# Performance work log

Measured on AMD Instinct MI355X. Metric: run time of the kernel, lower is better.

Reference implementation:

```python
import jax, jax.numpy as jnp
import numpy as np

B, N, V, H, R, A, IN, K = 64, 512, 64, 512, 4, 18, 128, 32
EPS = 1e-8


def setup_inputs() -> dict:
    key = jax.random.key(0)
    ks = jax.random.split(key, 20)
    g = lambda i, shape, s=1.0: jax.random.normal(ks[i], shape, jnp.float32) * s
    u = lambda i, shape: jax.random.uniform(ks[i], shape, dtype=jnp.float32)
    cin = IN + R * V
    return dict(
        x=g(0, (B, IN)),
        h=g(1, (B, H), 0.1),
        c=g(2, (B, H), 0.1),
        memory=g(3, (B, N, V), 0.1),
        read_weights=u(4, (B, R, N)),
        write_weights=u(5, (B, N)),
        usage=u(6, (B, N)),
        link_matrix=u(7, (B, N, N)) * 0.01,
        precedence_weights=u(8, (B, N)),
        W_ih=g(9, (4 * H, cin), 0.05), W_hh=g(10, (4 * H, H), 0.05),
        b_ih=jnp.zeros(4 * H, jnp.float32), b_hh=jnp.zeros(4 * H, jnp.float32),
        W_read=g(11, (R, V + 4, H), 0.05), b_read=jnp.zeros((R, V + 4), jnp.float32),
        W_write=g(12, (3 * V + 3, H), 0.05), b_write=jnp.zeros(3 * V + 3, jnp.float32),
        W_pol=g(13, (A, H), 0.05), b_pol=jnp.zeros(A, jnp.float32),
        W_val=g(14, (1, H), 0.05), b_val=jnp.zeros(1, jnp.float32),
    )


def reference(x, h, c, memory, read_weights, write_weights, usage, link_matrix,
              precedence_weights, W_ih, W_hh, b_ih, b_hh, W_read, b_read,
              W_write, b_write, W_pol, b_pol, W_val, b_val):
    # ---- read heads (vectorized over R) ----
    ro = jnp.einsum('roh,bh->bro', W_read, h) + b_read            # [B,R,V+4]
    rkey = ro[..., :V]
    rbeta = jax.nn.softplus(ro[..., V])                           # [B,R]
    rpi = jax.nn.softmax(ro[..., V + 1:V + 4], axis=-1)           # backward/content/forward gates
    mem_norm = jnp.maximum(jnp.linalg.norm(memory, axis=-1), EPS)  # [B,N]
    key_norm = jnp.maximum(jnp.linalg.norm(rkey, axis=-1), EPS)    # [B,R]
    sim = jnp.einsum('bnv,brv->brn', memory, rkey) / (mem_norm[:, None, :] * key_norm[..., None])
    scores = rbeta[..., None] * sim                                # [B,R,N]
    kth = jax.lax.top_k(scores, K)[0][..., -1:]                    # sparse top-k mask
    cw = jax.nn.softmax(jnp.where(scores >= kth, scores, -jnp.inf), axis=-1)
    fw = jnp.einsum('bnm,brm->brn', link_matrix, read_weights)     # forward weighting L w
    bw = jnp.einsum('bmn,brm->brn', link_matrix, read_weights)     # backward weighting L^T w
    w_r = rpi[..., 0:1] * bw + rpi[..., 1:2] * cw + rpi[..., 2:3] * fw  # [B,R,N]
    rvec = jnp.einsum('brn,bnv->brv', w_r, memory).reshape(B, R * V)
    # ---- LSTM controller (torch LSTMCell gate order i,f,g,o) ----
    gates = jnp.concatenate([x, rvec], -1) @ W_ih.T + h @ W_hh.T + b_ih + b_hh
    i_g, f_g, g_g, o_g = jnp.split(gates, 4, axis=-1)
    c_new = jax.nn.sigmoid(f_g) * c + jax.nn.sigmoid(i_g) * jnp.tanh(g_g)
    h_new = jax.nn.sigmoid(o_g) * jnp.tanh(c_new)
    # ---- write head ----
    wo = h_new @ W_write.T + b_write                               # [B,3V+3]
    wkey = wo[:, :V]
    erase = jax.nn.sigmoid(wo[:, V:2 * V])
    add = jnp.tanh(wo[:, 2 * V:3 * V])
    wbeta = jax.nn.softplus(wo[:, 3 * V])
    g_a = jax.nn.sigmoid(wo[:, 3 * V + 1])
    g_w = jax.nn.sigmoid(wo[:, 3 * V + 2])
    wkey_norm = jnp.maximum(jnp.linalg.norm(wkey, axis=-1), EPS)
    wsim = jnp.einsum('bnv,bv->bn', memory, wkey) / (mem_norm * wkey_norm[:, None])
    cw_w = jax.nn.softmax(wbeta[:, None] * wsim, axis=-1)
    # allocation weighting from sorted usage (DNC Eq. 1)
    idx = jnp.argsort(usage, axis=-1)
    u_sorted = jnp.take_along_axis(usage, idx, -1)
    prod_prev = jnp.concatenate([jnp.ones((B, 1), usage.dtype), jnp.cumprod(u_sorted, -1)[:, :-1]], -1)
    a_sorted = (1.0 - u_sorted) * prod_prev
    alloc = jnp.take_along_axis(a_sorted, jnp.argsort(idx, -1), -1)
    write_w = g_w[:, None] * (g_a[:, None] * alloc + (1.0 - g_a)[:, None] * cw_w)  # [B,N]
    # ---- memory erase/add ----
    mem_new = memory * (1.0 - write_w[:, :, None] * erase[:, None, :]) + write_w[:, :, None] * add[:, None, :]
    # ---- usage (psi detached as in torch.no_grad) ----
    psi = jax.lax.stop_gradient(jnp.prod(1.0 - w_r, axis=1))
    usage_new = (usage + write_weights - usage * write_weights) * psi
    # ---- link matrix + precedence ----
    ws = jnp.sum(write_w, -1, keepdims=True)
    prec_new = (1.0 - ws) * precedence_weights + write_w
    decay = (1.0 - write_w[:, :, None]) * (1.0 - write_w[:, None, :])
    link_new = decay * link_matrix + write_w[:, :, None] * precedence_weights[:, None, :]
    link_new = link_new * (1.0 - jnp.eye(N, dtype=link_new.dtype))
    # ---- actor/critic heads ----
    logits = h_new @ W_pol.T + b_pol
    value = h_new @ W_val.T + b_val
    return (logits, value, h_new, c_new, mem_new, w_r, write_w, usage_new, link_new, prec_new)
```

## Files before the change

kernel.cpp:

```cpp
#include <hip/hip_runtime.h>
#include <math.h>

constexpr int Bb = 64, Nn = 512, Vv = 64, Hh = 512, Rr = 4, Aa = 18, INp = 128, KTOP = 32;
constexpr int CIN = 384;
constexpr int ROo = 68;
constexpr int WOUT = 195;
#define EPSf 1e-8f

__device__ __forceinline__ float sigmoidf(float x){ return 1.f/(1.f+expf(-x)); }
__device__ __forceinline__ float softplusf(float x){ return (x>20.f)? x : log1pf(expf(x)); }
__device__ __forceinline__ float wave_reduce(float v){
  #pragma unroll
  for(int o=32;o>0;o>>=1) v += __shfl_down(v, o, 64);
  return v;
}

__global__ void k_read_proj(const float* __restrict__ Wr, const float* __restrict__ br,
                            const float* __restrict__ h, float* __restrict__ ro) {
  int bid = blockIdx.x;
  int b = bid / 68;
  int p = (bid % 68) * 4 + (threadIdx.x >> 6);
  int lane = threadIdx.x & 63;
  const float* wrow = Wr + p * Hh;
  const float* hb = h + b * Hh;
  float acc = 0.f;
  #pragma unroll
  for (int t = 0; t < 8; ++t) { int k = lane + 64*t; acc += wrow[k] * hb[k]; }
  acc = wave_reduce(acc);
  if (lane == 0) ro[b*272 + p] = acc + br[p];
}

__global__ void k_read_xform(const float* __restrict__ ro, float* __restrict__ rbeta,
                             float* __restrict__ rpi, float* __restrict__ keynorm) {
  int b = blockIdx.x;
  int r = threadIdx.x >> 6, lane = threadIdx.x & 63;
  const float* rob = ro + b*272 + r*ROo;
  float kv = rob[lane];
  float ssq = wave_reduce(kv*kv);
  if (lane == 0) {
    keynorm[b*Rr + r] = fmaxf(sqrtf(ssq), EPSf);
    rbeta[b*Rr + r] = softplusf(rob[64]);
    float e0 = rob[65], e1 = rob[66], e2 = rob[67];
    float m = fmaxf(e0, fmaxf(e1, e2));
    float x0 = expf(e0-m), x1 = expf(e1-m), x2 = expf(e2-m);
    float s = x0+x1+x2;
    rpi[(b*Rr+r)*3+0] = x0/s;
    rpi[(b*Rr+r)*3+1] = x1/s;
    rpi[(b*Rr+r)*3+2] = x2/s;
  }
}

__global__ void k_memnorm(const float* __restrict__ mem, float* __restrict__ memnorm) {
  int row = blockIdx.x * 4 + (threadIdx.x >> 6);
  int lane = threadIdx.x & 63;
  float m = mem[row*Vv + lane];
  float ssq = wave_reduce(m*m);
  if (lane == 0) memnorm[row] = fmaxf(sqrtf(ssq), EPSf);
}

__global__ void k_scores(const float* __restrict__ mem, const float* __restrict__ ro,
                         const float* __restrict__ rbeta, const float* __restrict__ keynorm,
                         const float* __restrict__ memnorm, float* __restrict__ scores) {
  int row = blockIdx.x*4 + (threadIdx.x>>6);
  int lane = threadIdx.x & 63;
  int b = row >> 9, n = row & 511;
  float m = mem[row*Vv + lane];
  float mn = memnorm[row];
  #pragma unroll
  for (int r = 0; r < Rr; ++r) {
    float p = m * ro[b*272 + r*ROo + lane];
    float s = wave_reduce(p);
    if (lane == 0)
      scores[(b*Rr + r)*Nn + n] = rbeta[b*Rr+r] * s / (mn * keynorm[b*Rr+r]);
  }
}

__global__ void k_topk_cw(const float* __restrict__ scores, float* __restrict__ cw) {
  __shared__ float sv[512];
  __shared__ float so[512];
  __shared__ float red[256];
  int br = blockIdx.x;
  int tid = threadIdx.x;
  const float* srow = scores + br*Nn;
  for (int i = tid; i < 512; i += 256) { float v = srow[i]; sv[i]=v; so[i]=v; }
  __syncthreads();
  for (int k = 2; k <= 512; k <<= 1) {
    for (int j = k>>1; j > 0; j >>= 1) {
      for (int i = tid; i < 512; i += 256) {
        int ixj = i ^ j;
        if (ixj > i) {
          float a = sv[i], c = sv[ixj];
          bool descSeg = ((i & k) == 0);
          bool sw = descSeg ? (a < c) : (a > c);
          if (sw) { sv[i]=c; sv[ixj]=a; }
        }
      }
      __syncthreads();
    }
  }
  float kth = sv[KTOP-1];
  float mx = sv[0];
  float lsum = 0.f;
  for (int i = tid; i < 512; i += 256) {
    float v = so[i];
    lsum += (v >= kth) ? expf(v - mx) : 0.f;
  }
  red[tid] = lsum; __syncthreads();
  for (int s2 = 128; s2 > 0; s2 >>= 1) {
    if (tid < s2) red[tid] += red[tid+s2];
    __syncthreads();
  }
  float inv = 1.f / red[0];
  for (int i = tid; i < 512; i += 256) {
    float v = so[i];
    cw[br*Nn + i] = (v >= kth) ? expf(v - mx)*inv : 0.f;
  }
}

__global__ void k_fw(const float* __restrict__ link, const float* __restrict__ rw,
                     float* __restrict__ fw) {
  int row = blockIdx.x*4 + (threadIdx.x>>6);
  int lane = threadIdx.x & 63;
  int b = row >> 9, n = row & 511;
  const float* lrow = link + (size_t)row * Nn;
  const float* rwb = rw + b*Rr*Nn;
  float a0=0,a1=0,a2=0,a3=0;
  #pragma unroll
  for (int t = 0; t < 8; ++t) {
    int k = lane + 64*t;
    float lv = lrow[k];
    a0 += lv * rwb[k];
    a1 += lv * rwb[Nn + k];
    a2 += lv * rwb[2*Nn + k];
    a3 += lv * rwb[3*Nn + k];
  }
  a0 = wave_reduce(a0); a1 = wave_reduce(a1);
  a2 = wave_reduce(a2); a3 = wave_reduce(a3);
  if (lane == 0) {
    fw[(b*Rr+0)*Nn+n] = a0;
    fw[(b*Rr+1)*Nn+n] = a1;
    fw[(b*Rr+2)*Nn+n] = a2;
    fw[(b*Rr+3)*Nn+n] = a3;
  }
}

__global__ void k_bw(const float* __restrict__ link, const float* __restrict__ rw,
                     float* __restrict__ bw) {
  __shared__ float lds[256*4];
  int b  = blockIdx.x >> 4;
  int jt = (blockIdx.x >> 2) & 3;
  int mc = blockIdx.x & 3;
  int tid = threadIdx.x;
  int j = jt*128 + (tid & 127);
  int half = tid >> 7;
  const float* lb = link + (size_t)b*Nn*Nn;
  const float* rwb = rw + b*Rr*Nn;
  float a0=0,a1=0,a2=0,a3=0;
  int m0 = mc*128 + half*64;
  for (int m = m0; m < m0+64; ++m) {
    float lv = lb[m*Nn + j];
    a0 += lv*rwb[m]; a1 += lv*rwb[Nn+m]; a2 += lv*rwb[2*Nn+m]; a3 += lv*rwb[3*Nn+m];
  }
  lds[tid*4+0]=a0; lds[tid*4+1]=a1; lds[tid*4+2]=a2; lds[tid*4+3]=a3;
  __syncthreads();
  if (tid < 128) {
    int jj = jt*128 + tid;
    #pragma unroll
    for (int r = 0; r < 4; ++r)
      atomicAdd(&bw[(b*Rr+r)*Nn + jj], lds[tid*4+r] + lds[(tid+128)*4+r]);
  }
}

__global__ void k_wr_usage(const float* __restrict__ bw, const float* __restrict__ cw,
                           const float* __restrict__ fw, const float* __restrict__ rpi,
                           const float* __restrict__ usage, const float* __restrict__ wwt,
                           float* __restrict__ out_wr, float* __restrict__ out_usage) {
  int idx = blockIdx.x*256 + threadIdx.x;
  int b = idx >> 9, n = idx & 511;
  float psi = 1.f;
  #pragma unroll
  for (int r = 0; r < Rr; ++r) {
    int br = b*Rr + r;
    float p0 = rpi[br*3], p1 = rpi[br*3+1], p2 = rpi[br*3+2];
    float w = p0*bw[br*Nn+n] + p1*cw[br*Nn+n] + p2*fw[br*Nn+n];
    out_wr[br*Nn+n] = w;
    psi *= (1.f - w);
  }
  float u = usage[idx], wt = wwt[idx];
  out_usage[idx] = (u + wt - u*wt) * psi;
}

__global__ void k_rvec(const float* __restrict__ wr, const float* __restrict__ mem,
                       float* __restrict__ rvec) {
  int b = blockIdx.x >> 3;
  int ch = blockIdx.x & 7;
  int r = threadIdx.x >> 6, v = threadIdx.x & 63;
  const float* wrow = wr + (b*Rr + r)*Nn;
  const float* mb = mem + (size_t)b*Nn*Vv;
  float acc = 0.f;
  #pragma unroll 4
  for (int t = 0; t < 64; ++t) {
    int n = ch*64 + t;
    acc += wrow[n] * mb[n*Vv + v];
  }
  atomicAdd(&rvec[(b*Rr+r)*Vv + v], acc);
}

__global__ void k_gates(const float* __restrict__ x, const float* __restrict__ rvec,
                        const float* __restrict__ h, const float* __restrict__ Wih,
                        const float* __restrict__ Whh, const float* __restrict__ bih,
                        const float* __restrict__ bhh, float* __restrict__ gates) {
  int gid = blockIdx.x*4 + (threadIdx.x>>6);
  int lane = threadIdx.x & 63;
  int j = gid >> 6, b = gid & 63;
  const float* wi = Wih + j*CIN;
  const float* wh = Whh + j*Hh;
  float acc = 0.f;
  #pragma unroll
  for (int t = 0; t < 6; ++t) {
    int k = lane + 64*t;
    float xin = (k < INp) ? x[b*INp + k] : rvec[b*(Rr*Vv) + k - INp];
    acc += xin * wi[k];
  }
  #pragma unroll
  for (int t = 0; t < 8; ++t) {
    int k = lane + 64*t;
    acc += h[b*Hh+k] * wh[k];
  }
  acc = wave_reduce(acc);
  if (lane == 0) gates[b*(4*Hh) + j] = acc + bih[j] + bhh[j];
}

__global__ void k_lstm(const float* __restrict__ gates, const float* __restrict__ c,
                       float* __restrict__ out_h, float* __restrict__ out_c) {
  int idx = blockIdx.x*256 + threadIdx.x;
  int b = idx >> 9, hh = idx & 511;
  const float* g = gates + b*2048;
  float ig = sigmoidf(g[hh]), fg = sigmoidf(g[512+hh]);
  float gg = tanhf(g[1024+hh]), og = sigmoidf(g[1536+hh]);
  float cn = fg * c[idx] + ig * gg;
  float hn = og * tanhf(cn);
  out_c[idx] = cn; out_h[idx] = hn;
}

__global__ void k_wo(const float* __restrict__ hn, const float* __restrict__ Ww,
                     const float* __restrict__ bw_, float* __restrict__ wo) {
  int gid = blockIdx.x*4 + (threadIdx.x>>6);
  int lane = threadIdx.x & 63;
  int b = gid / WOUT, o = gid % WOUT;
  const float* wrow = Ww + o*Hh;
  const float* hb = hn + b*Hh;
  float acc = 0.f;
  #pragma unroll
  for (int t = 0; t < 8; ++t) { int k = lane+64*t; acc += hb[k]*wrow[k]; }
  acc = wave_reduce(acc);
  if (lane==0) wo[b*WOUT+o] = acc + bw_[o];
}

__global__ void k_wknorm(const float* __restrict__ wo, float* __restrict__ wkn) {
  int b = blockIdx.x; int lane = threadIdx.x;
  float v = wo[b*WOUT + lane];
  float ssq = wave_reduce(v*v);
  if (lane==0) wkn[b] = fmaxf(sqrtf(ssq), EPSf);
}

__global__ void k_wsim(const float* __restrict__ mem, const float* __restrict__ wo,
                       const float* __restrict__ memnorm, const float* __restrict__ wkn,
                       float* __restrict__ wsim) {
  int row = blockIdx.x*4 + (threadIdx.x>>6);
  int lane = threadIdx.x & 63;
  int b = row >> 9, n = row & 511;
  const float* wob = wo + b*WOUT;
  float p = mem[row*Vv + lane] * wob[lane];
  float s = wave_reduce(p);
  if (lane == 0) {
    float wbeta = softplusf(wob[192]);
    wsim[row] = wbeta * s / (memnorm[row] * wkn[b]);
  }
}

__global__ void k_alloc(const float* __restrict__ usage, const float* __restrict__ wo,
                        const float* __restrict__ wsim, const float* __restrict__ prec,
                        float* __restrict__ out_ww, float* __restrict__ out_prec) {
  __shared__ float uv[512];
  __shared__ int   ui[512];
  __shared__ float cp[512];
  __shared__ float al[512];
  __shared__ float red[256];
  int b = blockIdx.x, tid = threadIdx.x;
  float s0 = wsim[b*Nn + tid], s1 = wsim[b*Nn + tid + 256];
  red[tid] = fmaxf(s0, s1); __syncthreads();
  for (int s2=128; s2>0; s2>>=1){ if (tid<s2) red[tid]=fmaxf(red[tid],red[tid+s2]); __syncthreads(); }
  float mx = red[0]; __syncthreads();
  float e0 = expf(s0-mx), e1 = expf(s1-mx);
  red[tid] = e0+e1; __syncthreads();
  for (int s2=128; s2>0; s2>>=1){ if (tid<s2) red[tid]+=red[tid+s2]; __syncthreads(); }
  float cinv = 1.f/red[0];
  float c0 = e0*cinv, c1 = e1*cinv;
  __syncthreads();
  for (int i = tid; i < 512; i += 256) { uv[i] = usage[b*Nn+i]; ui[i] = i; }
  __syncthreads();
  for (int k = 2; k <= 512; k <<= 1) {
    for (int j = k>>1; j > 0; j >>= 1) {
      for (int i = tid; i < 512; i += 256) {
        int ixj = i ^ j;
        if (ixj > i) {
          float av = uv[i], bv = uv[ixj];
          int ai = ui[i], bi = ui[ixj];
          bool gt = (av > bv) || (av == bv && ai > bi);
          bool asc = ((i & k) == 0);
          bool sw = asc ? gt : !gt;
          if (sw) { uv[i]=bv; uv[ixj]=av; ui[i]=bi; ui[ixj]=ai; }
        }
      }
      __syncthreads();
    }
  }
  for (int i = tid; i < 512; i += 256) cp[i] = uv[i];
  __syncthreads();
  for (int d = 1; d < 512; d <<= 1) {
    float t0 = cp[tid]     * ((tid >= d)     ? cp[tid-d]     : 1.f);
    float t1 = cp[tid+256] * ((tid+256 >= d) ? cp[tid+256-d] : 1.f);
    __syncthreads();
    cp[tid] = t0; cp[tid+256] = t1;
    __syncthreads();
  }
  for (int i = tid; i < 512; i += 256) {
    float pp = (i == 0) ? 1.f : cp[i-1];
    al[ui[i]] = (1.f - uv[i]) * pp;
  }
  __syncthreads();
  float ga = sigmoidf(wo[b*WOUT+193]);
  float gw = sigmoidf(wo[b*WOUT+194]);
  int n0 = tid, n1 = tid+256;
  float wv0 = gw * (ga*al[n0] + (1.f-ga)*c0);
  float wv1 = gw * (ga*al[n1] + (1.f-ga)*c1);
  out_ww[b*Nn+n0] = wv0; out_ww[b*Nn+n1] = wv1;
  red[tid] = wv0 + wv1; __syncthreads();
  for (int s2=128; s2>0; s2>>=1){ if (tid<s2) red[tid]+=red[tid+s2]; __syncthreads(); }
  float wsum = red[0];
  out_prec[b*Nn+n0] = (1.f - wsum)*prec[b*Nn+n0] + wv0;
  out_prec[b*Nn+n1] = (1.f - wsum)*prec[b*Nn+n1] + wv1;
}

__global__ void k_memnew(const float* __restrict__ mem, const float* __restrict__ wo,
                         const float* __restrict__ ww, float* __restrict__ out_mem) {
  int idx4 = blockIdx.x*256 + threadIdx.x;
  int base = idx4*4;
  int b = base >> 15;
  int rem = base & 32767;
  int n = rem >> 6;
  int v0 = rem & 63;
  float w = ww[b*Nn + n];
  const float* wob = wo + b*WOUT;
  float4 m = *(const float4*)(mem + base);
  float4 o;
  float e, a;
  e = sigmoidf(wob[64+v0+0]); a = tanhf(wob[128+v0+0]); o.x = m.x*(1.f-w*e)+w*a;
  e = sigmoidf(wob[64+v0+1]); a = tanhf(wob[128+v0+1]); o.y = m.y*(1.f-w*e)+w*a;
  e = sigmoidf(wob[64+v0+2]); a = tanhf(wob[128+v0+2]); o.z = m.z*(1.f-w*e)+w*a;
  e = sigmoidf(wob[64+v0+3]); a = tanhf(wob[128+v0+3]); o.w = m.w*(1.f-w*e)+w*a;
  *(float4*)(out_mem + base) = o;
}

__global__ void k_link(const float* __restrict__ link, const float* __restrict__ ww,
                       const float* __restrict__ prec, float* __restrict__ out_link) {
  int idx4 = blockIdx.x*256 + threadIdx.x;
  int base = idx4*4;
  int b = base >> 18;
  int rem = base & 262143;
  int i = rem >> 9;
  int j0 = rem & 511;
  float wi = ww[b*Nn + i];
  float fi = 1.f - wi;
  float4 lv = *(const float4*)(link + base);
  float4 wj = *(const float4*)(ww + b*Nn + j0);
  float4 pj = *(const float4*)(prec + b*Nn + j0);
  float4 o;
  o.x = fi*(1.f-wj.x)*lv.x + wi*pj.x;
  o.y = fi*(1.f-wj.y)*lv.y + wi*pj.y;
  o.z = fi*(1.f-wj.z)*lv.z + wi*pj.z;
  o.w = fi*(1.f-wj.w)*lv.w + wi*pj.w;
  if (i >= j0 && i < j0+4) {
    if (i == j0) o.x = 0.f;
    else if (i == j0+1) o.y = 0.f;
    else if (i == j0+2) o.z = 0.f;
    else o.w = 0.f;
  }
  *(float4*)(out_link + base) = o;
}

__global__ void k_polval(const float* __restrict__ hn, const float* __restrict__ Wp,
                         const float* __restrict__ bp, const float* __restrict__ Wv,
                         const float* __restrict__ bv, float* __restrict__ out_logits,
                         float* __restrict__ out_value) {
  int gid = blockIdx.x*4 + (threadIdx.x>>6);
  int lane = threadIdx.x & 63;
  int b = gid / 19, o = gid % 19;
  const float* hb = hn + b*Hh;
  const float* wrow = (o < Aa) ? (Wp + o*Hh) : Wv;
  float acc = 0.f;
  #pragma unroll
  for (int t = 0; t < 8; ++t) { int k = lane+64*t; acc += hb[k]*wrow[k]; }
  acc = wave_reduce(acc);
  if (lane == 0) {
    if (o < Aa) out_logits[b*Aa+o] = acc + bp[o];
    else out_value[b] = acc + bv[0];
  }
}

extern "C" void kernel_launch(void* const* d_in, const int* in_sizes, int n_in,
                              void* d_out, int out_size, void* d_ws, size_t ws_size,
                              hipStream_t stream) {
  const float* x    = (const float*)d_in[0];
  const float* h    = (const float*)d_in[1];
  const float* c    = (const float*)d_in[2];
  const float* mem  = (const float*)d_in[3];
  const float* rw   = (const float*)d_in[4];
  const float* wwt  = (const float*)d_in[5];
  const float* usage= (const float*)d_in[6];
  const float* link = (const float*)d_in[7];
  const float* prec = (const float*)d_in[8];
  const float* Wih  = (const float*)d_in[9];
  const float* Whh  = (const float*)d_in[10];
  const float* bih  = (const float*)d_in[11];
  const float* bhh  = (const float*)d_in[12];
  const float* Wr   = (const float*)d_in[13];
  const float* br   = (const float*)d_in[14];
  const float* Ww   = (const float*)d_in[15];
  const float* bw_  = (const float*)d_in[16];
  const float* Wp   = (const float*)d_in[17];
  const float* bp   = (const float*)d_in[18];
  const float* Wv   = (const float*)d_in[19];
  const float* bv   = (const float*)d_in[20];

  float* out = (float*)d_out;
  float* o_logits = out + 0;
  float* o_value  = out + 1152;
  float* o_h      = out + 1216;
  float* o_c      = out + 33984;
  float* o_mem    = out + 66752;
  float* o_wr     = out + 2163904;
  float* o_ww     = out + 2294976;
  float* o_usage  = out + 2327744;
  float* o_link   = out + 2360512;
  float* o_prec   = out + 19137728;

  float* ws = (float*)d_ws;
  float* ws_ro     = ws;
  float* ws_rbeta  = ws + 17408;
  float* ws_rpi    = ws + 17664;
  float* ws_kn     = ws + 18432;
  float* ws_mn     = ws + 18688;
  float* ws_sc     = ws + 51456;
  float* ws_cw     = ws + 182528;
  float* ws_fw     = ws + 313600;
  float* ws_bw     = ws + 444672;
  float* ws_rvec   = ws + 575744;
  float* ws_gates  = ws + 592128;
  float* ws_wo     = ws + 723200;
  float* ws_wkn    = ws + 735680;
  float* ws_wsim   = ws + 735744;

  hipMemsetAsync(ws_bw,   0, 131072*sizeof(float), stream);
  hipMemsetAsync(ws_rvec, 0, 16384*sizeof(float),  stream);

  k_read_proj <<<dim3(Bb*68),      dim3(256), 0, stream>>>(Wr, br, h, ws_ro);
  k_read_xform<<<dim3(Bb),         dim3(256), 0, stream>>>(ws_ro, ws_rbeta, ws_rpi, ws_kn);
  k_memnorm   <<<dim3(Bb*Nn/4),    dim3(256), 0, stream>>>(mem, ws_mn);
  k_scores    <<<dim3(Bb*Nn/4),    dim3(256), 0, stream>>>(mem, ws_ro, ws_rbeta, ws_kn, ws_mn, ws_sc);
  k_topk_cw   <<<dim3(Bb*Rr),      dim3(256), 0, stream>>>(ws_sc, ws_cw);
  k_fw        <<<dim3(Bb*Nn/4),    dim3(256), 0, stream>>>(link, rw, ws_fw);
  k_bw        <<<dim3(Bb*16),      dim3(256), 0, stream>>>(link, rw, ws_bw);
  k_wr_usage  <<<dim3(Bb*Nn/256),  dim3(256), 0, stream>>>(ws_bw, ws_cw, ws_fw, ws_rpi, usage, wwt, o_wr, o_usage);
  k_rvec      <<<dim3(Bb*8),       dim3(256), 0, stream>>>(o_wr, mem, ws_rvec);
  k_gates     <<<dim3(2048*Bb/4),  dim3(256), 0, stream>>>(x, ws_rvec, h, Wih, Whh, bih, bhh, ws_gates);
  k_lstm      <<<dim3(Bb*Hh/256),  dim3(256), 0, stream>>>(ws_gates, c, o_h, o_c);
  k_wo        <<<dim3(Bb*WOUT/4),  dim3(256), 0, stream>>>(o_h, Ww, bw_, ws_wo);
  k_wknorm    <<<dim3(Bb),         dim3(64),  0, stream>>>(ws_wo, ws_wkn);
  k_wsim      <<<dim3(Bb*Nn/4),    dim3(256), 0, stream>>>(mem, ws_wo, ws_mn, ws_wkn, ws_wsim);
  k_alloc     <<<dim3(Bb),         dim3(256), 0, stream>>>(usage, ws_wo, ws_wsim, prec, o_ww, o_prec);
  k_memnew    <<<dim3(Bb*Nn*Vv/1024), dim3(256), 0, stream>>>(mem, ws_wo, o_ww, o_mem);
  k_link      <<<dim3(Bb*Nn*Nn/1024), dim3(256), 0, stream>>>(link, o_ww, prec, o_link);
  k_polval    <<<dim3(Bb*19/4),    dim3(256), 0, stream>>>(o_h, Wp, bp, Wv, bv, o_logits, o_value);
}
```

Baseline: 356.4 us.

## Fuse small kernels, merge fw/bw link passes, and register-tile LSTM gate GEMV

Folds the norm, softplus and gate-softmax transforms into their consumer kernels, so k_read_xform, k_memnorm and k_wknorm go away. Forward and backward link weightings now come from one pass over the link matrix, with per-chunk backward partials replacing atomics and the two memsets. The gates GEMV is tiled 4x4 over (gate row, batch) per wave to reuse loads. The policy/value heads are merged into the write-output projection, and the memory and link update kernels are merged into one launch. This cuts launch count and the second read of the 64MB link tensor, at the cost of redundant reductions, more registers in k_fwbw, and an 8-way partial sum in k_wr_usage.

```diff
diff --git a/kernel.cpp b/kernel.cpp
--- a/kernel.cpp
+++ b/kernel.cpp
@@ -3,7 +3,6 @@
 
 constexpr int Bb = 64, Nn = 512, Vv = 64, Hh = 512, Rr = 4, Aa = 18, INp = 128, KTOP = 32;
 constexpr int CIN = 384;
-constexpr int ROo = 68;
 constexpr int WOUT = 195;
 #define EPSf 1e-8f
 
@@ -30,48 +29,25 @@
   if (lane == 0) ro[b*272 + p] = acc + br[p];
 }
 
-__global__ void k_read_xform(const float* __restrict__ ro, float* __restrict__ rbeta,
-                             float* __restrict__ rpi, float* __restrict__ keynorm) {
-  int b = blockIdx.x;
-  int r = threadIdx.x >> 6, lane = threadIdx.x & 63;
-  const float* rob = ro + b*272 + r*ROo;
-  float kv = rob[lane];
-  float ssq = wave_reduce(kv*kv);
-  if (lane == 0) {
-    keynorm[b*Rr + r] = fmaxf(sqrtf(ssq), EPSf);
-    rbeta[b*Rr + r] = softplusf(rob[64]);
-    float e0 = rob[65], e1 = rob[66], e2 = rob[67];
-    float m = fmaxf(e0, fmaxf(e1, e2));
-    float x0 = expf(e0-m), x1 = expf(e1-m), x2 = expf(e2-m);
-    float s = x0+x1+x2;
-    rpi[(b*Rr+r)*3+0] = x0/s;
-    rpi[(b*Rr+r)*3+1] = x1/s;
-    rpi[(b*Rr+r)*3+2] = x2/s;
-  }
-}
-
-__global__ void k_memnorm(const float* __restrict__ mem, float* __restrict__ memnorm) {
-  int row = blockIdx.x * 4 + (threadIdx.x >> 6);
-  int lane = threadIdx.x & 63;
-  float m = mem[row*Vv + lane];
-  float ssq = wave_reduce(m*m);
-  if (lane == 0) memnorm[row] = fmaxf(sqrtf(ssq), EPSf);
-}
-
 __global__ void k_scores(const float* __restrict__ mem, const float* __restrict__ ro,
-                         const float* __restrict__ rbeta, const float* __restrict__ keynorm,
-                         const float* __restrict__ memnorm, float* __restrict__ scores) {
+                         float* __restrict__ scores) {
   int row = blockIdx.x*4 + (threadIdx.x>>6);
   int lane = threadIdx.x & 63;
   int b = row >> 9, n = row & 511;
   float m = mem[row*Vv + lane];
-  float mn = memnorm[row];
+  float mn = wave_reduce(m*m);
   #pragma unroll
   for (int r = 0; r < Rr; ++r) {
-    float p = m * ro[b*272 + r*ROo + lane];
-    float s = wave_reduce(p);
-    if (lane == 0)
-      scores[(b*Rr + r)*Nn + n] = rbeta[b*Rr+r] * s / (mn * keynorm[b*Rr+r]);
+    const float* rob = ro + b*272 + r*68;
+    float kv = rob[lane];
+    float s  = wave_reduce(m*kv);
+    float k2 = wave_reduce(kv*kv);
+    if (lane == 0) {
+      float rbeta = softplusf(rob[64]);
+      float mnc = fmaxf(sqrtf(mn), EPSf);
+      float knc = fmaxf(sqrtf(k2), EPSf);
+      scores[(b*Rr + r)*Nn + n] = rbeta * s / (mnc * knc);
+    }
   }
 }
 
@@ -117,72 +93,78 @@
   }
 }
 
-__global__ void k_fw(const float* __restrict__ link, const float* __restrict__ rw,
-                     float* __restrict__ fw) {
-  int row = blockIdx.x*4 + (threadIdx.x>>6);
-  int lane = threadIdx.x & 63;
-  int b = row >> 9, n = row & 511;
-  const float* lrow = link + (size_t)row * Nn;
+__global__ void k_fwbw(const float* __restrict__ link, const float* __restrict__ rw,
+                       float* __restrict__ fw, float* __restrict__ bwpart) {
+  __shared__ float bl[4][4][512];
+  int b  = blockIdx.x >> 3;
+  int ch = blockIdx.x & 7;
+  int wv = threadIdx.x >> 6, lane = threadIdx.x & 63;
   const float* rwb = rw + b*Rr*Nn;
-  float a0=0,a1=0,a2=0,a3=0;
-  #pragma unroll
-  for (int t = 0; t < 8; ++t) {
-    int k = lane + 64*t;
-    float lv = lrow[k];
-    a0 += lv * rwb[k];
-    a1 += lv * rwb[Nn + k];
-    a2 += lv * rwb[2*Nn + k];
-    a3 += lv * rwb[3*Nn + k];
-  }
-  a0 = wave_reduce(a0); a1 = wave_reduce(a1);
-  a2 = wave_reduce(a2); a3 = wave_reduce(a3);
-  if (lane == 0) {
-    fw[(b*Rr+0)*Nn+n] = a0;
-    fw[(b*Rr+1)*Nn+n] = a1;
-    fw[(b*Rr+2)*Nn+n] = a2;
-    fw[(b*Rr+3)*Nn+n] = a3;
-  }
-}
-
-__global__ void k_bw(const float* __restrict__ link, const float* __restrict__ rw,
-                     float* __restrict__ bw) {
-  __shared__ float lds[256*4];
-  int b  = blockIdx.x >> 4;
-  int jt = (blockIdx.x >> 2) & 3;
-  int mc = blockIdx.x & 3;
+  float rwv[4][8];
+  #pragma unroll
+  for (int r = 0; r < 4; ++r)
+    #pragma unroll
+    for (int t = 0; t < 8; ++t) rwv[r][t] = rwb[r*512 + lane + 64*t];
+  float bwacc[8][4] = {};
+  const float* lb = link + (size_t)b*Nn*Nn;
+  int n0 = ch*64 + wv*16;
+  for (int i = 0; i < 16; ++i) {
+    int n = n0 + i;
+    float lk[8];
+    #pragma unroll
+    for (int t = 0; t < 8; ++t) lk[t] = lb[n*512 + lane + 64*t];
+    float s0 = rwb[n], s1 = rwb[512+n], s2 = rwb[1024+n], s3 = rwb[1536+n];
+    float f0=0,f1=0,f2=0,f3=0;
+    #pragma unroll
+    for (int t = 0; t < 8; ++t) {
+      float lv = lk[t];
+      f0 += lv*rwv[0][t]; f1 += lv*rwv[1][t]; f2 += lv*rwv[2][t]; f3 += lv*rwv[3][t];
+      bwacc[t][0] += lv*s0; bwacc[t][1] += lv*s1; bwacc[t][2] += lv*s2; bwacc[t][3] += lv*s3;
+    }
+    f0 = wave_reduce(f0); f1 = wave_reduce(f1);
+    f2 = wave_reduce(f2); f3 = wave_reduce(f3);
+    if (lane == 0) {
+      fw[(b*Rr+0)*Nn+n] = f0; fw[(b*Rr+1)*Nn+n] = f1;
+      fw[(b*Rr+2)*Nn+n] = f2; fw[(b*Rr+3)*Nn+n] = f3;
+    }
+  }
+  #pragma unroll
+  for (int t = 0; t < 8; ++t)
+    #pragma unroll
+    for (int r = 0; r < 4; ++r) bl[wv][r][lane + 64*t] = bwacc[t][r];
+  __syncthreads();
   int tid = threadIdx.x;
-  int j = jt*128 + (tid & 127);
-  int half = tid >> 7;
-  const float* lb = link + (size_t)b*Nn*Nn;
-  const float* rwb = rw + b*Rr*Nn;
-  float a0=0,a1=0,a2=0,a3=0;
-  int m0 = mc*128 + half*64;
-  for (int m = m0; m < m0+64; ++m) {
-    float lv = lb[m*Nn + j];
-    a0 += lv*rwb[m]; a1 += lv*rwb[Nn+m]; a2 += lv*rwb[2*Nn+m]; a3 += lv*rwb[3*Nn+m];
-  }
-  lds[tid*4+0]=a0; lds[tid*4+1]=a1; lds[tid*4+2]=a2; lds[tid*4+3]=a3;
-  __syncthreads();
-  if (tid < 128) {
-    int jj = jt*128 + tid;
-    #pragma unroll
-    for (int r = 0; r < 4; ++r)
-      atomicAdd(&bw[(b*Rr+r)*Nn + jj], lds[tid*4+r] + lds[(tid+128)*4+r]);
-  }
-}
-
-__global__ void k_wr_usage(const float* __restrict__ bw, const float* __restrict__ cw,
-                           const float* __restrict__ fw, const float* __restrict__ rpi,
+  #pragma unroll
+  for (int q = 0; q < 8; ++q) {
+    int idx = q*256 + tid;
+    int r = idx >> 9, j = idx & 511;
+    float v = bl[0][r][j] + bl[1][r][j] + bl[2][r][j] + bl[3][r][j];
+    bwpart[((size_t)(ch*Bb + b)*Rr + r)*Nn + j] = v;
+  }
+}
+
+__global__ void k_wr_usage(const float* __restrict__ bwpart, const float* __restrict__ cw,
+                           const float* __restrict__ fw, const float* __restrict__ ro,
                            const float* __restrict__ usage, const float* __restrict__ wwt,
-                           float* __restrict__ out_wr, float* __restrict__ out_usage) {
+                           float* __restrict__ out_wr, float* __restrict__ out_usage,
+                           float* __restrict__ ws_rvec) {
   int idx = blockIdx.x*256 + threadIdx.x;
+  if (idx < Bb*Rr*Vv) ws_rvec[idx] = 0.f;
   int b = idx >> 9, n = idx & 511;
   float psi = 1.f;
   #pragma unroll
   for (int r = 0; r < Rr; ++r) {
     int br = b*Rr + r;
-    float p0 = rpi[br*3], p1 = rpi[br*3+1], p2 = rpi[br*3+2];
-    float w = p0*bw[br*Nn+n] + p1*cw[br*Nn+n] + p2*fw[br*Nn+n];
+    const float* rob = ro + b*272 + r*68;
+    float e0 = rob[65], e1 = rob[66], e2 = rob[67];
+    float m = fmaxf(e0, fmaxf(e1, e2));
+    float x0 = expf(e0-m), x1 = expf(e1-m), x2 = expf(e2-m);
+    float inv = 1.f/(x0+x1+x2);
+    float bwv = 0.f;
+    #pragma unroll
+    for (int chh = 0; chh < 8; ++chh)
+      bwv += bwpart[((size_t)(chh*Bb + b)*Rr + r)*Nn + n];
+    float w = (x0*bwv + x1*cw[br*Nn+n] + x2*fw[br*Nn+n]) * inv;
     out_wr[br*Nn+n] = w;
     psi *= (1.f - w);
   }
@@ -212,23 +194,48 @@
                         const float* __restrict__ bhh, float* __restrict__ gates) {
   int gid = blockIdx.x*4 + (threadIdx.x>>6);
   int lane = threadIdx.x & 63;
-  int j = gid >> 6, b = gid & 63;
-  const float* wi = Wih + j*CIN;
-  const float* wh = Whh + j*Hh;
-  float acc = 0.f;
+  int jt = gid >> 4;
+  int bt = gid & 15;
+  float acc[4][4] = {};
   #pragma unroll
   for (int t = 0; t < 6; ++t) {
     int k = lane + 64*t;
-    float xin = (k < INp) ? x[b*INp + k] : rvec[b*(Rr*Vv) + k - INp];
-    acc += xin * wi[k];
+    float u[4], w[4];
+    #pragma unroll
+    for (int i = 0; i < 4; ++i) {
+      int b = bt*4 + i;
+      u[i] = (k < INp) ? x[b*INp + k] : rvec[b*(Rr*Vv) + k - INp];
+      w[i] = Wih[(jt*4+i)*CIN + k];
+    }
+    #pragma unroll
+    for (int jj = 0; jj < 4; ++jj)
+      #pragma unroll
+      for (int bb = 0; bb < 4; ++bb) acc[jj][bb] += w[jj]*u[bb];
   }
   #pragma unroll
   for (int t = 0; t < 8; ++t) {
     int k = lane + 64*t;
-    acc += h[b*Hh+k] * wh[k];
-  }
-  acc = wave_reduce(acc);
-  if (lane == 0) gates[b*(4*Hh) + j] = acc + bih[j] + bhh[j];
+    float u[4], w[4];
+    #pragma unroll
+    for (int i = 0; i < 4; ++i) {
+      u[i] = h[(bt*4+i)*Hh + k];
+      w[i] = Whh[(jt*4+i)*Hh + k];
+    }
+    #pragma unroll
+    for (int jj = 0; jj < 4; ++jj)
+      #pragma unroll
+      for (int bb = 0; bb < 4; ++bb) acc[jj][bb] += w[jj]*u[bb];
+  }
+  #pragma unroll
+  for (int jj = 0; jj < 4; ++jj)
+    #pragma unroll
+    for (int bb = 0; bb < 4; ++bb) {
+      float v = wave_reduce(acc[jj][bb]);
+      if (lane == 0) {
+        int j = jt*4 + jj, b = bt*4 + bb;
+        gates[b*(4*Hh) + j] = v + bih[j] + bhh[j];
+      }
+    }
 }
 
 __global__ void k_lstm(const float* __restrict__ gates, const float* __restrict__ c,
@@ -243,39 +250,44 @@
   out_c[idx] = cn; out_h[idx] = hn;
 }
 
-__global__ void k_wo(const float* __restrict__ hn, const float* __restrict__ Ww,
-                     const float* __restrict__ bw_, float* __restrict__ wo) {
+__global__ void k_wopol(const float* __restrict__ hn, const float* __restrict__ Ww,
+                        const float* __restrict__ bw_, const float* __restrict__ Wp,
+                        const float* __restrict__ bp, const float* __restrict__ Wv,
+                        const float* __restrict__ bv, float* __restrict__ wo,
+                        float* __restrict__ out_logits, float* __restrict__ out_value) {
   int gid = blockIdx.x*4 + (threadIdx.x>>6);
   int lane = threadIdx.x & 63;
-  int b = gid / WOUT, o = gid % WOUT;
-  const float* wrow = Ww + o*Hh;
+  int b = gid / 214, o = gid % 214;
+  const float* wrow;
+  if (o < WOUT) wrow = Ww + o*Hh;
+  else if (o < WOUT + Aa) wrow = Wp + (o-WOUT)*Hh;
+  else wrow = Wv;
   const float* hb = hn + b*Hh;
   float acc = 0.f;
   #pragma unroll
   for (int t = 0; t < 8; ++t) { int k = lane+64*t; acc += hb[k]*wrow[k]; }
   acc = wave_reduce(acc);
-  if (lane==0) wo[b*WOUT+o] = acc + bw_[o];
-}
-
-__global__ void k_wknorm(const float* __restrict__ wo, float* __restrict__ wkn) {
-  int b = blockIdx.x; int lane = threadIdx.x;
-  float v = wo[b*WOUT + lane];
-  float ssq = wave_reduce(v*v);
-  if (lane==0) wkn[b] = fmaxf(sqrtf(ssq), EPSf);
+  if (lane == 0) {
+    if (o < WOUT) wo[b*WOUT+o] = acc + bw_[o];
+    else if (o < WOUT + Aa) out_logits[b*Aa + (o-WOUT)] = acc + bp[o-WOUT];
+    else out_value[b] = acc + bv[0];
+  }
 }
 
 __global__ void k_wsim(const float* __restrict__ mem, const float* __restrict__ wo,
-                       const float* __restrict__ memnorm, const float* __restrict__ wkn,
                        float* __restrict__ wsim) {
   int row = blockIdx.x*4 + (threadIdx.x>>6);
   int lane = threadIdx.x & 63;
-  int b = row >> 9, n = row & 511;
+  int b = row >> 9;
   const float* wob = wo + b*WOUT;
-  float p = mem[row*Vv + lane] * wob[lane];
-  float s = wave_reduce(p);
+  float kv = wob[lane];
+  float m = mem[row*Vv + lane];
+  float s  = wave_reduce(m*kv);
+  float mn = wave_reduce(m*m);
+  float k2 = wave_reduce(kv*kv);
   if (lane == 0) {
     float wbeta = softplusf(wob[192]);
-    wsim[row] = wbeta * s / (memnorm[row] * wkn[b]);
+    wsim[row] = wbeta * s / (fmaxf(sqrtf(mn),EPSf) * fmaxf(sqrtf(k2),EPSf));
   }
 }
 
@@ -343,69 +355,52 @@
   out_prec[b*Nn+n1] = (1.f - wsum)*prec[b*Nn+n1] + wv1;
 }
 
-__global__ void k_memnew(const float* __restrict__ mem, const float* __restrict__ wo,
-                         const float* __restrict__ ww, float* __restrict__ out_mem) {
-  int idx4 = blockIdx.x*256 + threadIdx.x;
-  int base = idx4*4;
-  int b = base >> 15;
-  int rem = base & 32767;
-  int n = rem >> 6;
-  int v0 = rem & 63;
-  float w = ww[b*Nn + n];
-  const float* wob = wo + b*WOUT;
-  float4 m = *(const float4*)(mem + base);
-  float4 o;
-  float e, a;
-  e = sigmoidf(wob[64+v0+0]); a = tanhf(wob[128+v0+0]); o.x = m.x*(1.f-w*e)+w*a;
-  e = sigmoidf(wob[64+v0+1]); a = tanhf(wob[128+v0+1]); o.y = m.y*(1.f-w*e)+w*a;
-  e = sigmoidf(wob[64+v0+2]); a = tanhf(wob[128+v0+2]); o.z = m.z*(1.f-w*e)+w*a;
-  e = sigmoidf(wob[64+v0+3]); a = tanhf(wob[128+v0+3]); o.w = m.w*(1.f-w*e)+w*a;
-  *(float4*)(out_mem + base) = o;
-}
-
-__global__ void k_link(const float* __restrict__ link, const float* __restrict__ ww,
-                       const float* __restrict__ prec, float* __restrict__ out_link) {
-  int idx4 = blockIdx.x*256 + threadIdx.x;
-  int base = idx4*4;
-  int b = base >> 18;
-  int rem = base & 262143;
-  int i = rem >> 9;
-  int j0 = rem & 511;
-  float wi = ww[b*Nn + i];
-  float fi = 1.f - wi;
-  float4 lv = *(const float4*)(link + base);
-  float4 wj = *(const float4*)(ww + b*Nn + j0);
-  float4 pj = *(const float4*)(prec + b*Nn + j0);
-  float4 o;
-  o.x = fi*(1.f-wj.x)*lv.x + wi*pj.x;
-  o.y = fi*(1.f-wj.y)*lv.y + wi*pj.y;
-  o.z = fi*(1.f-wj.z)*lv.z + wi*pj.z;
-  o.w = fi*(1.f-wj.w)*lv.w + wi*pj.w;
-  if (i >= j0 && i < j0+4) {
-    if (i == j0) o.x = 0.f;
-    else if (i == j0+1) o.y = 0.f;
-    else if (i == j0+2) o.z = 0.f;
-    else o.w = 0.f;
-  }
-  *(float4*)(out_link + base) = o;
-}
-
-__global__ void k_polval(const float* __restrict__ hn, const float* __restrict__ Wp,
-                         const float* __restrict__ bp, const float* __restrict__ Wv,
-                         const float* __restrict__ bv, float* __restrict__ out_logits,
-                         float* __restrict__ out_value) {
-  int gid = blockIdx.x*4 + (threadIdx.x>>6);
-  int lane = threadIdx.x & 63;
-  int b = gid / 19, o = gid % 19;
-  const float* hb = hn + b*Hh;
-  const float* wrow = (o < Aa) ? (Wp + o*Hh) : Wv;
-  float acc = 0.f;
-  #pragma unroll
-  for (int t = 0; t < 8; ++t) { int k = lane+64*t; acc += hb[k]*wrow[k]; }
-  acc = wave_reduce(acc);
-  if (lane == 0) {
-    if (o < Aa) out_logits[b*Aa+o] = acc + bp[o];
-    else out_value[b] = acc + bv[0];
+__global__ void k_memlink(const float* __restrict__ link, const float* __restrict__ ww,
+                          const float* __restrict__ prec, const float* __restrict__ mem,
+                          const float* __restrict__ wo, float* __restrict__ out_link,
+                          float* __restrict__ out_mem) {
+  int bid = blockIdx.x;
+  if (bid < 16384) {
+    int idx4 = bid*256 + threadIdx.x;
+    int base = idx4*4;
+    int b = base >> 18;
+    int rem = base & 262143;
+    int i = rem >> 9;
+    int j0 = rem & 511;
+    float wi = ww[b*Nn + i];
+    float fi = 1.f - wi;
+    float4 lv = *(const float4*)(link + base);
+    float4 wj = *(const float4*)(ww + b*Nn + j0);
+    float4 pj = *(const float4*)(prec + b*Nn + j0);
+    float4 o;
+    o.x = fi*(1.f-wj.x)*lv.x + wi*pj.x;
+    o.y = fi*(1.f-wj.y)*lv.y + wi*pj.y;
+    o.z = fi*(1.f-wj.z)*lv.z + wi*pj.z;
+    o.w = fi*(1.f-wj.w)*lv.w + wi*pj.w;
+    if (i >= j0 && i < j0+4) {
+      if (i == j0) o.x = 0.f;
+      else if (i == j0+1) o.y = 0.f;
+      else if (i == j0+2) o.z = 0.f;
+      else o.w = 0.f;
+    }
+    *(float4*)(out_link + base) = o;
+  } else {
+    int idx4 = (bid - 16384)*256 + threadIdx.x;
+    int base = idx4*4;
+    int b = base >> 15;
+    int rem = base & 32767;
+    int n = rem >> 6;
+    int v0 = rem & 63;
+    float w = ww[b*Nn + n];
+    const float* wob = wo + b*WOUT;
+    float4 m = *(const float4*)(mem + base);
+    float4 o;
+    float e, a;
+    e = sigmoidf(wob[64+v0+0]); a = tanhf(wob[128+v0+0]); o.x = m.x*(1.f-w*e)+w*a;
+    e = sigmoidf(wob[64+v0+1]); a = tanhf(wob[128+v0+1]); o.y = m.y*(1.f-w*e)+w*a;
+    e = sigmoidf(wob[64+v0+2]); a = tanhf(wob[128+v0+2]); o.z = m.z*(1.f-w*e)+w*a;
+    e = sigmoidf(wob[64+v0+3]); a = tanhf(wob[128+v0+3]); o.w = m.w*(1.f-w*e)+w*a;
+    *(float4*)(out_mem + base) = o;
   }
 }
 
@@ -448,39 +443,25 @@
 
   float* ws = (float*)d_ws;
   float* ws_ro     = ws;
-  float* ws_rbeta  = ws + 17408;
-  float* ws_rpi    = ws + 17664;
-  float* ws_kn     = ws + 18432;
-  float* ws_mn     = ws + 18688;
-  float* ws_sc     = ws + 51456;
-  float* ws_cw     = ws + 182528;
-  float* ws_fw     = ws + 313600;
-  float* ws_bw     = ws + 444672;
-  float* ws_rvec   = ws + 575744;
-  float* ws_gates  = ws + 592128;
-  float* ws_wo     = ws + 723200;
-  float* ws_wkn    = ws + 735680;
-  float* ws_wsim   = ws + 735744;
-
-  hipMemsetAsync(ws_bw,   0, 131072*sizeof(float), stream);
-  hipMemsetAsync(ws_rvec, 0, 16384*sizeof(float),  stream);
-
-  k_read_proj <<<dim3(Bb*68),      dim3(256), 0, stream>>>(Wr, br, h, ws_ro);
-  k_read_xform<<<dim3(Bb),         dim3(256), 0, stream>>>(ws_ro, ws_rbeta, ws_rpi, ws_kn);
-  k_memnorm   <<<dim3(Bb*Nn/4),    dim3(256), 0, stream>>>(mem, ws_mn);
-  k_scores    <<<dim3(Bb*Nn/4),    dim3(256), 0, stream>>>(mem, ws_ro, ws_rbeta, ws_kn, ws_mn, ws_sc);
-  k_topk_cw   <<<dim3(Bb*Rr),      dim3(256), 0, stream>>>(ws_sc, ws_cw);
-  k_fw        <<<dim3(Bb*Nn/4),    dim3(256), 0, stream>>>(link, rw, ws_fw);
-  k_bw        <<<dim3(Bb*16),      dim3(256), 0, stream>>>(link, rw, ws_bw);
-  k_wr_usage  <<<dim3(Bb*Nn/256),  dim3(256), 0, stream>>>(ws_bw, ws_cw, ws_fw, ws_rpi, usage, wwt, o_wr, o_usage);
-  k_rvec      <<<dim3(Bb*8),       dim3(256), 0, stream>>>(o_wr, mem, ws_rvec);
-  k_gates     <<<dim3(2048*Bb/4),  dim3(256), 0, stream>>>(x, ws_rvec, h, Wih, Whh, bih, bhh, ws_gates);
-  k_lstm      <<<dim3(Bb*Hh/256),  dim3(256), 0, stream>>>(ws_gates, c, o_h, o_c);
-  k_wo        <<<dim3(Bb*WOUT/4),  dim3(256), 0, stream>>>(o_h, Ww, bw_, ws_wo);
-  k_wknorm    <<<dim3(Bb),         dim3(64),  0, stream>>>(ws_wo, ws_wkn);
-  k_wsim      <<<dim3(Bb*Nn/4),    dim3(256), 0, stream>>>(mem, ws_wo, ws_mn, ws_wkn, ws_wsim);
-  k_alloc     <<<dim3(Bb),         dim3(256), 0, stream>>>(usage, ws_wo, ws_wsim, prec, o_ww, o_prec);
-  k_memnew    <<<dim3(Bb*Nn*Vv/1024), dim3(256), 0, stream>>>(mem, ws_wo, o_ww, o_mem);
-  k_link      <<<dim3(Bb*Nn*Nn/1024), dim3(256), 0, stream>>>(link, o_ww, prec, o_link);
-  k_polval    <<<dim3(Bb*19/4),    dim3(256), 0, stream>>>(o_h, Wp, bp, Wv, bv, o_logits, o_value);
-}
+  float* ws_sc     = ws + 17408;
+  float* ws_cw     = ws + 148480;
+  float* ws_fw     = ws + 279552;
+  float* ws_bwpart = ws + 410624;
+  float* ws_rvec   = ws + 1459200;
+  float* ws_gates  = ws + 1475584;
+  float* ws_wo     = ws + 1606656;
+  float* ws_wsim   = ws + 1619136;
+
+  k_read_proj <<<dim3(Bb*68),        dim3(256), 0, stream>>>(Wr, br, h, ws_ro);
+  k_scores    <<<dim3(Bb*Nn/4),      dim3(256), 0, stream>>>(mem, ws_ro, ws_sc);
+  k_topk_cw   <<<dim3(Bb*Rr),        dim3(256), 0, stream>>>(ws_sc, ws_cw);
+  k_fwbw      <<<dim3(Bb*8),         dim3(256), 0, stream>>>(link, rw, ws_fw, ws_bwpart);
+  k_wr_usage  <<<dim3(Bb*Nn/256),    dim3(256), 0, stream>>>(ws_bwpart, ws_cw, ws_fw, ws_ro, usage, wwt, o_wr, o_usage, ws_rvec);
+  k_rvec      <<<dim3(Bb*8),         dim3(256), 0, stream>>>(o_wr, mem, ws_rvec);
+  k_gates     <<<dim3(2048),         dim3(256), 0, stream>>>(x, ws_rvec, h, Wih, Whh, bih, bhh, ws_gates);
+  k_lstm      <<<dim3(Bb*Hh/256),    dim3(256), 0, stream>>>(ws_gates, c, o_h, o_c);
+  k_wopol     <<<dim3(Bb*214/4),     dim3(256), 0, stream>>>(o_h, Ww, bw_, Wp, bp, Wv, bv, ws_wo, o_logits, o_value);
+  k_wsim      <<<dim3(Bb*Nn/4),      dim3(256), 0, stream>>>(mem, ws_wo, ws_wsim);
+  k_alloc     <<<dim3(Bb),           dim3(256), 0, stream>>>(usage, ws_wo, ws_wsim, prec, o_ww, o_prec);
+  k_memlink   <<<dim3(16384+2048),   dim3(256), 0, stream>>>(link, o_ww, prec, mem, ws_wo, o_link, o_mem);
+}
```

After: 345.2 us. 1.03x faster.
